# Performance work log

Measured on AMD Instinct MI355X. Metric: run time of the kernel, lower is better.

The kernel has to match this reference:

```python
import jax, jax.numpy as jnp
import numpy as np

D_MODEL = 1024
N_HEADS = 16
HEAD_DIM = D_MODEL // N_HEADS
D_FF = 4096
ROPE_RANK = 16
LN_EPS = 1e-5


def _ln(x, g, b):
    mu = jnp.mean(x, axis=-1, keepdims=True)
    var = jnp.mean((x - mu) ** 2, axis=-1, keepdims=True)
    return (x - mu) * jax.lax.rsqrt(var + LN_EPS) * g + b


def _rope(x, A, B_):
    # x: [B, T, D]; learned low-rank additive correction to sin/cos tables
    B, T, D = x.shape
    pos = jnp.arange(T, dtype=jnp.float32)
    theta = 1.0 / (10000.0 ** (jnp.arange(0, D, 2, dtype=jnp.float32) / D))  # [D/2]
    angles = pos[:, None] * theta[None, :]                                   # [T, D/2]
    sin_pos, cos_pos = jnp.sin(angles), jnp.cos(angles)
    base = jnp.concatenate([sin_pos, cos_pos], axis=-1)                      # [T, D]
    learned = (base @ A) @ B_                                                # [T, D]
    l_sin, l_cos = jnp.split(learned, 2, axis=-1)
    sin_f = sin_pos + l_sin                                                  # [T, D/2]
    cos_f = cos_pos + l_cos
    xe, xo = x[..., ::2], x[..., 1::2]
    re = xe * cos_f[None] - xo * sin_f[None]
    ro = xe * sin_f[None] + xo * cos_f[None]
    return jnp.stack([re, ro], axis=-1).reshape(B, T, D)


def setup_inputs() -> dict:
    key = jax.random.key(0)
    ks = jax.random.split(key, 20)
    B, T = 2, 2048
    s = 1.0 / np.sqrt(D_MODEL)
    sf = 1.0 / np.sqrt(D_FF)
    sr = 1.0 / np.sqrt(ROPE_RANK)
    return {
        "tgt": jax.random.normal(ks[0], (B, T, D_MODEL), jnp.float32),
        "Wq": jax.random.normal(ks[1], (D_MODEL, D_MODEL), jnp.float32) * s,
        "bq": jnp.zeros((D_MODEL,), jnp.float32),
        "Wk": jax.random.normal(ks[2], (D_MODEL, D_MODEL), jnp.float32) * s,
        "bk": jnp.zeros((D_MODEL,), jnp.float32),
        "Wv": jax.random.normal(ks[3], (D_MODEL, D_MODEL), jnp.float32) * s,
        "bv": jnp.zeros((D_MODEL,), jnp.float32),
        "Wo": jax.random.normal(ks[4], (D_MODEL, D_MODEL), jnp.float32) * s,
        "bo": jnp.zeros((D_MODEL,), jnp.float32),
        "W1": jax.random.normal(ks[5], (D_MODEL, D_FF), jnp.float32) * s,
        "b1": jnp.zeros((D_FF,), jnp.float32),
        "W2": jax.random.normal(ks[6], (D_FF, D_MODEL), jnp.float32) * sf,
        "b2": jnp.zeros((D_MODEL,), jnp.float32),
        "ln1_g": jnp.ones((D_MODEL,), jnp.float32),
        "ln1_b": jnp.zeros((D_MODEL,), jnp.float32),
        "ln2_g": jnp.ones((D_MODEL,), jnp.float32),
        "ln2_b": jnp.zeros((D_MODEL,), jnp.float32),
        "rope_A": jax.random.normal(ks[7], (D_MODEL, ROPE_RANK), jnp.float32) * s,
        "rope_B": jax.random.normal(ks[8], (ROPE_RANK, D_MODEL), jnp.float32) * sr,
    }


def reference(tgt, Wq, bq, Wk, bk, Wv, bv, Wo, bo, W1, b1, W2, b2,
              ln1_g, ln1_b, ln2_g, ln2_b, rope_A, rope_B):
    x = tgt
    B, T, D = x.shape
    q = _rope(x @ Wq + bq, rope_A, rope_B)
    k = _rope(x @ Wk + bk, rope_A, rope_B)
    v = x @ Wv + bv
    # [B, H, T, hd]
    q = q.reshape(B, T, N_HEADS, HEAD_DIM).transpose(0, 2, 1, 3)
    k = k.reshape(B, T, N_HEADS, HEAD_DIM).transpose(0, 2, 1, 3)
    v = v.reshape(B, T, N_HEADS, HEAD_DIM).transpose(0, 2, 1, 3)
    scores = jnp.einsum("bhqd,bhkd->bhqk", q, k) / np.sqrt(HEAD_DIM)
    attn = jax.nn.softmax(scores, axis=-1)  # no mask: module applies none
    ctx = jnp.einsum("bhqk,bhkd->bhqd", attn, v)
    ctx = ctx.transpose(0, 2, 1, 3).reshape(B, T, D)
    x = x + (ctx @ Wo + bo)
    x = _ln(x, ln1_g, ln1_b)
    ff = jax.nn.relu(x @ W1 + b1) @ W2 + b2
    x = _ln(x + ff, ln2_g, ln2_b)
    return x
```

## Files before the change

### kernel.cpp

```cpp
#include <hip/hip_runtime.h>
#include <math.h>

typedef unsigned short u16;
typedef unsigned int u32;
typedef __attribute__((ext_vector_type(8))) short short8v;
typedef __attribute__((ext_vector_type(4))) float f32x4;

__device__ __forceinline__ u16 f2bf(float f) {
    u32 u = __float_as_uint(f);
    u32 r = (u + 0x7fffu + ((u >> 16) & 1u)) >> 16;
    return (u16)r;
}

#define GLOAD_LDS(g, l)                                                        \
    __builtin_amdgcn_global_load_lds(                                          \
        (const __attribute__((address_space(1))) void*)(g),                    \
        (__attribute__((address_space(3))) void*)(l), 16, 0, 0)

__global__ void cast_k(const float* __restrict__ x, u16* __restrict__ y) {
    const int gid = blockIdx.x * blockDim.x + threadIdx.x;
    float4 v = ((const float4*)x)[gid];
    ushort4 o;
    o.x = f2bf(v.x); o.y = f2bf(v.y); o.z = f2bf(v.z); o.w = f2bf(v.w);
    ((ushort4*)y)[gid] = o;
}

__global__ __launch_bounds__(256) void tcast_k(const float* __restrict__ S,
                                               u16* __restrict__ Dt,
                                               int K, int N) {
    __shared__ float tile[32][33];
    const int n0 = blockIdx.x * 32, k0 = blockIdx.y * 32;
    const int tx = threadIdx.x & 31, ty = threadIdx.x >> 5;
#pragma unroll
    for (int i = 0; i < 4; i++)
        tile[ty + 8 * i][tx] = S[(size_t)(k0 + ty + 8 * i) * N + n0 + tx];
    __syncthreads();
#pragma unroll
    for (int i = 0; i < 4; i++)
        Dt[(size_t)(n0 + ty + 8 * i) * K + k0 + tx] = f2bf(tile[tx][ty + 8 * i]);
}

__global__ __launch_bounds__(256) void vtrans_k(const u16* __restrict__ vv,
                                                u16* __restrict__ Vt) {
    __shared__ u16 tile[32][33];
    const int key0 = blockIdx.x * 32, d0 = blockIdx.y * 32, bh = blockIdx.z;
    const int b = bh >> 4, h = bh & 15;
    const int tx = threadIdx.x & 31, ty = threadIdx.x >> 5;
#pragma unroll
    for (int i = 0; i < 4; i++)
        tile[ty + 8 * i][tx] =
            vv[(size_t)(b * 2048 + key0 + ty + 8 * i) * 1024 + h * 64 + d0 + tx];
    __syncthreads();
#pragma unroll
    for (int i = 0; i < 4; i++) {
        const int d = d0 + ty + 8 * i;
        const int key = key0 + tx;
        const int ksw = (key & ~63) | ((((key >> 3) & 7) ^ (d & 7)) << 3) | (key & 7);
        Vt[((size_t)bh * 64 + d) * 2048 + ksw] = tile[tx][ty + 8 * i];
    }
}

#define ROPE_LOG2C (13.287712379549449f / 512.0f)

__global__ __launch_bounds__(256) void rope1_k(const float* __restrict__ A,
                                               float* __restrict__ P) {
    __shared__ float sc[16][17];
    __shared__ float cc[16][17];
    __shared__ float Als[16][17];
    __shared__ float Alc[16][17];
    const int tid = threadIdx.x;
    const int tt = tid >> 4, rr = tid & 15;
    const int t = blockIdx.x * 16 + tt;
    float acc = 0.f;
    for (int i0 = 0; i0 < 512; i0 += 16) {
        __syncthreads();
        {
            const int i = i0 + rr;
            const float th = exp2f(-(float)i * ROPE_LOG2C);
            const float ang = (float)t * th;
            sc[tt][rr] = sinf(ang);
            cc[tt][rr] = cosf(ang);
            Als[tt][rr] = A[(i0 + tt) * 16 + rr];
            Alc[tt][rr] = A[(512 + i0 + tt) * 16 + rr];
        }
        __syncthreads();
#pragma unroll
        for (int ii = 0; ii < 16; ++ii)
            acc = fmaf(sc[tt][ii], Als[ii][rr],
                       fmaf(cc[tt][ii], Alc[ii][rr], acc));
    }
    P[t * 16 + rr] = acc;
}

__global__ void rope2_k(const float* __restrict__ P, const float* __restrict__ Bw,
                        float* __restrict__ sf, float* __restrict__ cf) {
    const int gid = blockIdx.x * blockDim.x + threadIdx.x;
    if (gid >= 2048 * 512) return;
    const int t = gid >> 9, i = gid & 511;
    float ls = 0.f, lc = 0.f;
#pragma unroll
    for (int r = 0; r < 16; ++r) {
        const float p = P[t * 16 + r];
        ls = fmaf(p, Bw[r * 1024 + i], ls);
        lc = fmaf(p, Bw[r * 1024 + 512 + i], lc);
    }
    const float th = exp2f(-(float)i * ROPE_LOG2C);
    const float ang = (float)t * th;
    sf[gid] = sinf(ang) + ls;
    cf[gid] = cosf(ang) + lc;
}

__device__ __forceinline__ void xcd_tile(int L, int xn, int rn, int rm,
                                         int& tm, int& tn) {
    const int xcd = L & 7, i = L >> 3;
    const int cx = xcd % xn, cy = xcd / xn;
    tn = cx * rn + (i % rn);
    tm = cy * rm + (i / rn);
}

enum { EP_NONE = 0, EP_RES = 2, EP_RELU = 3 };

template <int EPI, bool CBF, int BN>
__global__ __launch_bounds__(256) void mgemm_k(
    const u16* __restrict__ A, const u16* __restrict__ Bt,
    const float* __restrict__ bias, const float* __restrict__ resf,
    void* __restrict__ Cp, int M, int N, int K, int xn, int rn, int rm) {
    constexpr int NT = BN / 32;
    __shared__ u16 As[2 * 128 * 32];
    __shared__ u16 Bs[2 * BN * 32];
    const int tid = threadIdx.x;
    const int w = tid >> 6, l = tid & 63;
    const int quad = l >> 4, lr = l & 15;
    const int wr = w >> 1, wc = w & 1;
    int tm, tn;
    xcd_tile(blockIdx.x, xn, rn, rm, tm, tn);
    const int m0 = tm * 128, n0 = tn * BN;

    const int srow = w * 16 + (l >> 2);
    const int scol = (l & 3) * 8;
    const u16* ag0 = A + (size_t)(m0 + srow) * K + scol;
    const u16* ag1 = A + (size_t)(m0 + 64 + srow) * K + scol;
    const u16* bg0 = Bt + (size_t)(n0 + srow) * K + scol;
    const u16* bg1 = Bt + (size_t)(n0 + 64 + srow) * K + scol;

    f32x4 acc[4][NT];
#pragma unroll
    for (int i = 0; i < 4; i++)
#pragma unroll
        for (int j = 0; j < NT; j++) acc[i][j] = (f32x4)(0.0f);

    {
        u16* Ab = As;
        u16* Bb = Bs;
        GLOAD_LDS(ag0, Ab + w * 512);
        GLOAD_LDS(ag1, Ab + 2048 + w * 512);
        GLOAD_LDS(bg0, Bb + w * 512);
        if (BN == 128) GLOAD_LDS(bg1, Bb + 2048 + w * 512);
    }

    const int niter = K >> 5;
    for (int i = 0; i < niter; ++i) {
        __syncthreads();
        const int knext = (i + 1) << 5;
        if (knext < K) {
            u16* Ab = As + ((i + 1) & 1) * 4096;
            u16* Bb = Bs + ((i + 1) & 1) * (BN * 32);
            GLOAD_LDS(ag0 + knext, Ab + w * 512);
            GLOAD_LDS(ag1 + knext, Ab + 2048 + w * 512);
            GLOAD_LDS(bg0 + knext, Bb + w * 512);
            if (BN == 128) GLOAD_LDS(bg1 + knext, Bb + 2048 + w * 512);
        }
        const u16* Ac = As + (i & 1) * 4096;
        const u16* Bc = Bs + (i & 1) * (BN * 32);
        short8v af[4], bf[NT];
#pragma unroll
        for (int mt = 0; mt < 4; ++mt)
            af[mt] = *(const short8v*)&Ac[(wr * 64 + mt * 16 + lr) * 32 + quad * 8];
#pragma unroll
        for (int nt = 0; nt < NT; ++nt)
            bf[nt] = *(const short8v*)&Bc[(wc * (BN / 2) + nt * 16 + lr) * 32 + quad * 8];
#pragma unroll
        for (int mt = 0; mt < 4; ++mt)
#pragma unroll
            for (int nt = 0; nt < NT; ++nt)
                acc[mt][nt] = __builtin_amdgcn_mfma_f32_16x16x32_bf16(
                    af[mt], bf[nt], acc[mt][nt], 0, 0, 0);
    }

#pragma unroll
    for (int mt = 0; mt < 4; ++mt) {
#pragma unroll
        for (int nt = 0; nt < NT; ++nt) {
            const int n = n0 + wc * (BN / 2) + nt * 16 + lr;
            const float bb = bias[n];
#pragma unroll
            for (int reg = 0; reg < 4; ++reg) {
                const int m = m0 + wr * 64 + mt * 16 + quad * 4 + reg;
                float v = acc[mt][nt][reg] + bb;
                if (EPI == EP_RES) v += resf[(size_t)m * N + n];
                if (EPI == EP_RELU) v = fmaxf(v, 0.f);
                if (CBF) ((u16*)Cp)[(size_t)m * N + n] = f2bf(v);
                else     ((float*)Cp)[(size_t)m * N + n] = v;
            }
        }
    }
}

__global__ __launch_bounds__(256) void mqkv_k(
    const u16* __restrict__ A, const u16* __restrict__ Bt,
    const float* __restrict__ bq, const float* __restrict__ bk,
    const float* __restrict__ bv, const float* __restrict__ sf,
    const float* __restrict__ cf, u16* __restrict__ out) {
    const int K = 1024;
    __shared__ u16 As[2 * 128 * 32];
    __shared__ u16 Bs[2 * 128 * 32];
    const int tid = threadIdx.x;
    const int w = tid >> 6, l = tid & 63;
    const int quad = l >> 4, lr = l & 15;
    const int wr = w >> 1, wc = w & 1;
    int tm, tn;
    xcd_tile(blockIdx.x, 4, 6, 16, tm, tn);
    const int m0 = tm * 128, n0 = tn * 128;

    const int srow = w * 16 + (l >> 2);
    const int scol = (l & 3) * 8;
    const u16* ag0 = A + (size_t)(m0 + srow) * K + scol;
    const u16* ag1 = A + (size_t)(m0 + 64 + srow) * K + scol;
    const u16* bg0 = Bt + (size_t)(n0 + srow) * K + scol;
    const u16* bg1 = Bt + (size_t)(n0 + 64 + srow) * K + scol;

    f32x4 acc[4][4];
#pragma unroll
    for (int i = 0; i < 4; i++)
#pragma unroll
        for (int j = 0; j < 4; j++) acc[i][j] = (f32x4)(0.0f);

    {
        GLOAD_LDS(ag0, As + w * 512);
        GLOAD_LDS(ag1, As + 2048 + w * 512);
        GLOAD_LDS(bg0, Bs + w * 512);
        GLOAD_LDS(bg1, Bs + 2048 + w * 512);
    }
    for (int i = 0; i < 32; ++i) {
        __syncthreads();
        const int knext = (i + 1) << 5;
        if (knext < K) {
            u16* Ab = As + ((i + 1) & 1) * 4096;
            u16* Bb = Bs + ((i + 1) & 1) * 4096;
            GLOAD_LDS(ag0 + knext, Ab + w * 512);
            GLOAD_LDS(ag1 + knext, Ab + 2048 + w * 512);
            GLOAD_LDS(bg0 + knext, Bb + w * 512);
            GLOAD_LDS(bg1 + knext, Bb + 2048 + w * 512);
        }
        const u16* Ac = As + (i & 1) * 4096;
        const u16* Bc = Bs + (i & 1) * 4096;
        short8v af[4], bf[4];
#pragma unroll
        for (int mt = 0; mt < 4; ++mt)
            af[mt] = *(const short8v*)&Ac[(wr * 64 + mt * 16 + lr) * 32 + quad * 8];
#pragma unroll
        for (int nt = 0; nt < 4; ++nt)
            bf[nt] = *(const short8v*)&Bc[(wc * 64 + nt * 16 + lr) * 32 + quad * 8];
#pragma unroll
        for (int mt = 0; mt < 4; ++mt)
#pragma unroll
            for (int nt = 0; nt < 4; ++nt)
                acc[mt][nt] = __builtin_amdgcn_mfma_f32_16x16x32_bf16(
                    af[mt], bf[nt], acc[mt][nt], 0, 0, 0);
    }

    const int which = n0 >> 10;
    const float* bias = which == 0 ? bq : (which == 1 ? bk : bv);
    const bool doRope = which < 2;
    u16* Cp = out + (size_t)which * 4096 * 1024;

#pragma unroll
    for (int mt = 0; mt < 4; ++mt) {
#pragma unroll
        for (int nt = 0; nt < 4; ++nt) {
            const int n = n0 + wc * 64 + nt * 16 + lr;
            const int col = n & 1023;
            const float bb = bias[col];
#pragma unroll
            for (int reg = 0; reg < 4; ++reg) {
                const int m = m0 + wr * 64 + mt * 16 + quad * 4 + reg;
                float v = acc[mt][nt][reg] + bb;
                const float partner = __shfl_xor(v, 1);
                int colw = col;
                if (doRope) {
                    const int t = m & 2047;
                    const int fi = col >> 1;
                    const float svv = sf[t * 512 + fi];
                    const float cvv = cf[t * 512 + fi];
                    v = (col & 1) ? fmaf(partner, svv, v * cvv)
                                  : fmaf(v, cvv, -partner * svv);
                    if (which == 0) v *= 0.125f;
                    colw = (col & ~63) | ((((col >> 3) & 7) ^ (m & 7)) << 3) |
                           (col & 7);
                }
                Cp[(size_t)m * 1024 + colw] = f2bf(v);
            }
        }
    }
}

__global__ __launch_bounds__(256, 3) void mattn_k(
    const u16* __restrict__ Q, const u16* __restrict__ Kg,
    const u16* __restrict__ Vt, u16* __restrict__ O) {
    __shared__ u16 QPs[128 * 64];
    __shared__ u16 Ks[2][64 * 64];
    __shared__ u16 Vs[2][64 * 64];
    const int tid = threadIdx.x;
    const int w = tid >> 6, l = tid & 63;
    const int quad = l >> 4, lr = l & 15;
    const int L = blockIdx.x;
    const int bh = (L & 7) * 4 + ((L >> 3) & 3);
    const int b = bh >> 4, h = bh & 15;
    const int row0 = (L >> 5) * 128;
    const size_t base = (size_t)b * 2048 * 1024 + (size_t)h * 64;
    const size_t vbase = (size_t)bh * 64 * 2048;

    const int dr = l >> 3;
    const int dc = (l & 7) * 8;
    const int g0 = w * 2, g1 = g0 + 1;
    const u16* kg0 = Kg + base + (size_t)(g0 * 8 + dr) * 1024 + dc;
    const u16* kg1 = Kg + base + (size_t)(g1 * 8 + dr) * 1024 + dc;
    const u16* vg0 = Vt + vbase + (size_t)(g0 * 8 + dr) * 2048 + dc;
    const u16* vg1 = Vt + vbase + (size_t)(g1 * 8 + dr) * 2048 + dc;

#pragma unroll
    for (int j = 0; j < 4; ++j) {
        const int g = w * 4 + j;
        GLOAD_LDS(Q + base + (size_t)(row0 + g * 8 + dr) * 1024 + dc,
                  QPs + g * 512);
    }
    GLOAD_LDS(kg0, Ks[0] + g0 * 512);
    GLOAD_LDS(kg1, Ks[0] + g1 * 512);
    GLOAD_LDS(vg0, Vs[0] + g0 * 512);
    GLOAD_LDS(vg1, Vs[0] + g1 * 512);
    __syncthreads();

    const int rsw = lr & 7;
    short8v qf[2][2];
#pragma unroll
    for (int ntq = 0; ntq < 2; ++ntq) {
        const int qr = w * 32 + ntq * 16 + lr;
#pragma unroll
        for (int kh = 0; kh < 2; ++kh)
            qf[ntq][kh] = *(const short8v*)&QPs[qr * 64 +
                (((kh * 4 + quad) ^ rsw) << 3)];
    }

    f32x4 o_acc[2][4];
#pragma unroll
    for (int i = 0; i < 2; ++i)
#pragma unroll
        for (int j = 0; j < 4; ++j) o_acc[i][j] = (f32x4)(0.0f);
    float lsum[2] = {0.f, 0.f};

    for (int i = 0; i < 32; ++i) {
        __syncthreads();
        if (i + 1 < 32) {
            const size_t kro = (size_t)((i + 1) << 6) * 1024;
            const int kco = (i + 1) << 6;
            u16* Kb = Ks[(i + 1) & 1];
            u16* Vb = Vs[(i + 1) & 1];
            GLOAD_LDS(kg0 + kro, Kb + g0 * 512);
            GLOAD_LDS(kg1 + kro, Kb + g1 * 512);
            GLOAD_LDS(vg0 + kco, Vb + g0 * 512);
            GLOAD_LDS(vg1 + kco, Vb + g1 * 512);
        }
        const u16* Kc = Ks[i & 1];
        const u16* Vc = Vs[i & 1];

        f32x4 s[4][2];
#pragma unroll
        for (int mt = 0; mt < 4; ++mt)
#pragma unroll
            for (int ntq = 0; ntq < 2; ++ntq) s[mt][ntq] = (f32x4)(0.0f);
#pragma unroll
        for (int mt = 0; mt < 4; ++mt) {
            const int kr = mt * 16 + lr;
            const short8v kf0 = *(const short8v*)&Kc[kr * 64 + ((quad ^ rsw) << 3)];
            const short8v kf1 = *(const short8v*)&Kc[kr * 64 + (((quad + 4) ^ rsw) << 3)];
#pragma unroll
            for (int ntq = 0; ntq < 2; ++ntq) {
                s[mt][ntq] = __builtin_amdgcn_mfma_f32_16x16x32_bf16(
                    kf0, qf[ntq][0], s[mt][ntq], 0, 0, 0);
                s[mt][ntq] = __builtin_amdgcn_mfma_f32_16x16x32_bf16(
                    kf1, qf[ntq][1], s[mt][ntq], 0, 0, 0);
            }
        }

#pragma unroll
        for (int ntq = 0; ntq < 2; ++ntq) {
            const int prow = w * 32 + ntq * 16 + lr;
#pragma unroll
            for (int mt = 0; mt < 4; ++mt) {
                const float e0 = __expf(s[mt][ntq][0]);
                const float e1 = __expf(s[mt][ntq][1]);
                const float e2 = __expf(s[mt][ntq][2]);
                const float e3 = __expf(s[mt][ntq][3]);
                lsum[ntq] += (e0 + e1) + (e2 + e3);
                u32 p01, p23;
                asm("v_cvt_pk_bf16_f32 %0, %1, %2" : "=v"(p01) : "v"(e0), "v"(e1));
                asm("v_cvt_pk_bf16_f32 %0, %1, %2" : "=v"(p23) : "v"(e2), "v"(e3));
                uint2 pv; pv.x = p01; pv.y = p23;
                *(uint2*)&QPs[prow * 64 +
                              (((mt * 2 + (quad >> 1)) ^ rsw) << 3) +
                              (quad & 1) * 4] = pv;
            }
        }

        short8v vf[4][2];
#pragma unroll
        for (int ntd = 0; ntd < 4; ++ntd) {
            const int vr = ntd * 16 + lr;
            vf[ntd][0] = *(const short8v*)&Vc[vr * 64 + ((quad ^ rsw) << 3)];
            vf[ntd][1] = *(const short8v*)&Vc[vr * 64 + (((quad + 4) ^ rsw) << 3)];
        }
        short8v pf[2][2];
#pragma unroll
        for (int mtq = 0; mtq < 2; ++mtq) {
            const int prow = w * 32 + mtq * 16 + lr;
            pf[mtq][0] = *(const short8v*)&QPs[prow * 64 + ((quad ^ rsw) << 3)];
            pf[mtq][1] = *(const short8v*)&QPs[prow * 64 + (((quad + 4) ^ rsw) << 3)];
        }
#pragma unroll
        for (int mtq = 0; mtq < 2; ++mtq)
#pragma unroll
            for (int ntd = 0; ntd < 4; ++ntd) {
                o_acc[mtq][ntd] = __builtin_amdgcn_mfma_f32_16x16x32_bf16(
                    pf[mtq][0], vf[ntd][0], o_acc[mtq][ntd], 0, 0, 0);
                o_acc[mtq][ntd] = __builtin_amdgcn_mfma_f32_16x16x32_bf16(
                    pf[mtq][1], vf[ntd][1], o_acc[mtq][ntd], 0, 0, 0);
            }
    }

    float rden[2];
#pragma unroll
    for (int ntq = 0; ntq < 2; ++ntq) {
        float t = lsum[ntq];
        t += __shfl_xor(t, 16);
        t += __shfl_xor(t, 32);
        rden[ntq] = 1.0f / t;
    }
#pragma unroll
    for (int mtq = 0; mtq < 2; ++mtq) {
#pragma unroll
        for (int reg = 0; reg < 4; ++reg) {
            const float dsc = __shfl(rden[mtq], quad * 4 + reg);
            const int m = row0 + w * 32 + mtq * 16 + quad * 4 + reg;
#pragma unroll
            for (int ntd = 0; ntd < 4; ++ntd)
                O[base + (size_t)m * 1024 + ntd * 16 + lr] =
                    f2bf(o_acc[mtq][ntd][reg] * dsc);
        }
    }
}

__global__ __launch_bounds__(256) void ln_k(
    const float* __restrict__ X, const float* __restrict__ g,
    const float* __restrict__ bb, float* __restrict__ outf,
    u16* __restrict__ outb) {
    const int row = blockIdx.x, tid = threadIdx.x;
    const float* x = X + (size_t)row * 1024;
    float4 xv = *(const float4*)&x[tid * 4];
    float s = xv.x + xv.y + xv.z + xv.w;
    float s2 = xv.x * xv.x + xv.y * xv.y + xv.z * xv.z + xv.w * xv.w;
#pragma unroll
    for (int msk = 32; msk >= 1; msk >>= 1) {
        s += __shfl_xor(s, msk);
        s2 += __shfl_xor(s2, msk);
    }
    __shared__ float red[8];
    const int wv = tid >> 6;
    if ((tid & 63) == 0) { red[wv] = s; red[wv + 4] = s2; }
    __syncthreads();
    s = red[0] + red[1] + red[2] + red[3];
    s2 = red[4] + red[5] + red[6] + red[7];
    const float mu = s * (1.f / 1024.f);
    float var = s2 * (1.f / 1024.f) - mu * mu;
    var = fmaxf(var, 0.f);
    const float rstd = rsqrtf(var + 1e-5f);
    float4 g4 = *(const float4*)&g[tid * 4];
    float4 b4 = *(const float4*)&bb[tid * 4];
    float o0 = (xv.x - mu) * rstd * g4.x + b4.x;
    float o1 = (xv.y - mu) * rstd * g4.y + b4.y;
    float o2 = (xv.z - mu) * rstd * g4.z + b4.z;
    float o3 = (xv.w - mu) * rstd * g4.w + b4.w;
    if (outf)
        *(float4*)(outf + (size_t)row * 1024 + tid * 4) = make_float4(o0, o1, o2, o3);
    if (outb) {
        ushort4 ov;
        ov.x = f2bf(o0); ov.y = f2bf(o1); ov.z = f2bf(o2); ov.w = f2bf(o3);
        *(ushort4*)(outb + (size_t)row * 1024 + tid * 4) = ov;
    }
}

extern "C" void kernel_launch(void* const* d_in, const int* in_sizes, int n_in,
                              void* d_out, int out_size, void* d_ws, size_t ws_size,
                              hipStream_t stream) {
    const float* tgt = (const float*)d_in[0];
    const float* Wq  = (const float*)d_in[1];
    const float* bq  = (const float*)d_in[2];
    const float* Wk  = (const float*)d_in[3];
    const float* bk  = (const float*)d_in[4];
    const float* Wv  = (const float*)d_in[5];
    const float* bv  = (const float*)d_in[6];
    const float* Wo  = (const float*)d_in[7];
    const float* bo  = (const float*)d_in[8];
    const float* W1  = (const float*)d_in[9];
    const float* b1  = (const float*)d_in[10];
    const float* W2  = (const float*)d_in[11];
    const float* b2  = (const float*)d_in[12];
    const float* g1  = (const float*)d_in[13];
    const float* be1 = (const float*)d_in[14];
    const float* g2  = (const float*)d_in[15];
    const float* be2 = (const float*)d_in[16];
    const float* rA  = (const float*)d_in[17];
    const float* rB  = (const float*)d_in[18];

    const int M = 4096, D = 1024, DFF = 4096;
    const size_t MD = (size_t)M * D;
    const size_t MB = 1u << 20;
    char* wsb = (char*)d_ws;

    u16* q    = (u16*)wsb;
    u16* vv   = q + 2 * MD;
    u16* ctx  = q + 3 * MD;
    u16* h    = q;
    float* x1  = (float*)(wsb + 32 * MB);
    float* sfp = (float*)(wsb + 48 * MB);
    float* cfp = sfp + (size_t)2048 * 512;
    u16* x1b  = (u16*)sfp;
    u16* tgtb = (u16*)(wsb + 56 * MB);
    u16* Vt   = (u16*)(wsb + 56 * MB);
    u16* Wqt  = (u16*)(wsb + 64 * MB);
    u16* Wkt  = (u16*)(wsb + 66 * MB);
    u16* Wvt  = (u16*)(wsb + 68 * MB);
    u16* Wot  = (u16*)(wsb + 70 * MB);
    u16* W1t  = (u16*)(wsb + 72 * MB);
    u16* W2t  = (u16*)(wsb + 80 * MB);
    float* Pp = (float*)(wsb + 88 * MB);

    cast_k<<<dim3(4096), dim3(256), 0, stream>>>(tgt, tgtb);
    tcast_k<<<dim3(32, 32),  dim3(256), 0, stream>>>(Wq, Wqt, D, D);
    tcast_k<<<dim3(32, 32),  dim3(256), 0, stream>>>(Wk, Wkt, D, D);
    tcast_k<<<dim3(32, 32),  dim3(256), 0, stream>>>(Wv, Wvt, D, D);
    tcast_k<<<dim3(32, 32),  dim3(256), 0, stream>>>(Wo, Wot, D, D);
    tcast_k<<<dim3(128, 32), dim3(256), 0, stream>>>(W1, W1t, D, DFF);
    tcast_k<<<dim3(32, 128), dim3(256), 0, stream>>>(W2, W2t, DFF, D);
    rope1_k<<<dim3(128), dim3(256), 0, stream>>>(rA, Pp);
    rope2_k<<<dim3(4096), dim3(256), 0, stream>>>(Pp, rB, sfp, cfp);

    mqkv_k<<<dim3(768), dim3(256), 0, stream>>>(
        tgtb, Wqt, bq, bk, bv, sfp, cfp, q);

    vtrans_k<<<dim3(64, 2, 32), dim3(256), 0, stream>>>(vv, Vt);

    mattn_k<<<dim3(512), dim3(256), 0, stream>>>(q, q + MD, Vt, ctx);

    mgemm_k<EP_RES, false, 64><<<dim3(512), dim3(256), 0, stream>>>(
        ctx, Wot, bo, tgt, x1, M, D, D, 2, 8, 8);
    ln_k<<<dim3(4096), dim3(256), 0, stream>>>(x1, g1, be1, x1, x1b);
    mgemm_k<EP_RELU, true, 128><<<dim3(1024), dim3(256), 0, stream>>>(
        x1b, W1t, b1, nullptr, h, M, DFF, D, 4, 8, 16);
    mgemm_k<EP_RES, false, 64><<<dim3(512), dim3(256), 0, stream>>>(
        h, W2t, b2, x1, x1, M, D, DFF, 2, 8, 8);
    ln_k<<<dim3(4096), dim3(256), 0, stream>>>(x1, g2, be2, (float*)d_out, nullptr);

    (void)in_sizes; (void)n_in; (void)out_size; (void)ws_size;
}
```

Baseline: 459.4 us.

## Triple-buffer GEMM LDS stages with explicit waitcnt and XOR-swizzled LDS layout

```diff
diff --git a/kernel.cpp b/kernel.cpp
--- a/kernel.cpp
+++ b/kernel.cpp
@@ -16,6 +16,8 @@
     __builtin_amdgcn_global_load_lds(                                          \
         (const __attribute__((address_space(1))) void*)(g),                    \
         (__attribute__((address_space(3))) void*)(l), 16, 0, 0)
+
+#define SCHED_FENCE() __builtin_amdgcn_sched_barrier(0)
 
 __global__ void cast_k(const float* __restrict__ x, u16* __restrict__ y) {
     const int gid = blockIdx.x * blockDim.x + threadIdx.x;
@@ -126,8 +128,8 @@
     const float* __restrict__ bias, const float* __restrict__ resf,
     void* __restrict__ Cp, int M, int N, int K, int xn, int rn, int rm) {
     constexpr int NT = BN / 32;
-    __shared__ u16 As[2 * 128 * 32];
-    __shared__ u16 Bs[2 * BN * 32];
+    __shared__ u16 As[3 * 128 * 32];
+    __shared__ u16 Bs[3 * BN * 32];
     const int tid = threadIdx.x;
     const int w = tid >> 6, l = tid & 63;
     const int quad = l >> 4, lr = l & 15;
@@ -137,7 +139,7 @@
     const int m0 = tm * 128, n0 = tn * BN;
 
     const int srow = w * 16 + (l >> 2);
-    const int scol = (l & 3) * 8;
+    const int scol = (((l & 3) ^ ((l >> 3) & 3)) * 8);
     const u16* ag0 = A + (size_t)(m0 + srow) * K + scol;
     const u16* ag1 = A + (size_t)(m0 + 64 + srow) * K + scol;
     const u16* bg0 = Bt + (size_t)(n0 + srow) * K + scol;
@@ -150,41 +152,57 @@
         for (int j = 0; j < NT; j++) acc[i][j] = (f32x4)(0.0f);
 
     {
-        u16* Ab = As;
-        u16* Bb = Bs;
-        GLOAD_LDS(ag0, Ab + w * 512);
-        GLOAD_LDS(ag1, Ab + 2048 + w * 512);
-        GLOAD_LDS(bg0, Bb + w * 512);
-        if (BN == 128) GLOAD_LDS(bg1, Bb + 2048 + w * 512);
+        GLOAD_LDS(ag0, As + w * 512);
+        GLOAD_LDS(ag1, As + 2048 + w * 512);
+        GLOAD_LDS(bg0, Bs + w * 512);
+        if (BN == 128) GLOAD_LDS(bg1, Bs + 2048 + w * 512);
+        GLOAD_LDS(ag0 + 32, As + 4096 + w * 512);
+        GLOAD_LDS(ag1 + 32, As + 4096 + 2048 + w * 512);
+        GLOAD_LDS(bg0 + 32, Bs + BN * 32 + w * 512);
+        if (BN == 128) GLOAD_LDS(bg1 + 32, Bs + BN * 32 + 2048 + w * 512);
     }
 
     const int niter = K >> 5;
+    const int xsw = ((lr >> 1) & 3) << 3;
+    int bc = 0, bs = 2;
     for (int i = 0; i < niter; ++i) {
-        __syncthreads();
-        const int knext = (i + 1) << 5;
-        if (knext < K) {
-            u16* Ab = As + ((i + 1) & 1) * 4096;
-            u16* Bb = Bs + ((i + 1) & 1) * (BN * 32);
-            GLOAD_LDS(ag0 + knext, Ab + w * 512);
-            GLOAD_LDS(ag1 + knext, Ab + 2048 + w * 512);
-            GLOAD_LDS(bg0 + knext, Bb + w * 512);
-            if (BN == 128) GLOAD_LDS(bg1 + knext, Bb + 2048 + w * 512);
-        }
-        const u16* Ac = As + (i & 1) * 4096;
-        const u16* Bc = Bs + (i & 1) * (BN * 32);
+        SCHED_FENCE();
+        if (i + 1 < niter) {
+            if (BN == 128) asm volatile("s_waitcnt vmcnt(4) lgkmcnt(0)" ::: "memory");
+            else           asm volatile("s_waitcnt vmcnt(3) lgkmcnt(0)" ::: "memory");
+        } else {
+            asm volatile("s_waitcnt vmcnt(0) lgkmcnt(0)" ::: "memory");
+        }
+        __builtin_amdgcn_s_barrier();
+        SCHED_FENCE();
+        if (i + 2 < niter) {
+            const int kk = (i + 2) << 5;
+            u16* Ab = As + bs * 4096;
+            u16* Bb = Bs + bs * (BN * 32);
+            GLOAD_LDS(ag0 + kk, Ab + w * 512);
+            GLOAD_LDS(ag1 + kk, Ab + 2048 + w * 512);
+            GLOAD_LDS(bg0 + kk, Bb + w * 512);
+            if (BN == 128) GLOAD_LDS(bg1 + kk, Bb + 2048 + w * 512);
+        }
+        const u16* Ac = As + bc * 4096;
+        const u16* Bc = Bs + bc * (BN * 32);
         short8v af[4], bf[NT];
 #pragma unroll
         for (int mt = 0; mt < 4; ++mt)
-            af[mt] = *(const short8v*)&Ac[(wr * 64 + mt * 16 + lr) * 32 + quad * 8];
+            af[mt] = *(const short8v*)&Ac[(wr * 64 + mt * 16 + lr) * 32 +
+                                          ((quad << 3) ^ xsw)];
 #pragma unroll
         for (int nt = 0; nt < NT; ++nt)
-            bf[nt] = *(const short8v*)&Bc[(wc * (BN / 2) + nt * 16 + lr) * 32 + quad * 8];
+            bf[nt] = *(const short8v*)&Bc[(wc * (BN / 2) + nt * 16 + lr) * 32 +
+                                          ((quad << 3) ^ xsw)];
 #pragma unroll
         for (int mt = 0; mt < 4; ++mt)
 #pragma unroll
             for (int nt = 0; nt < NT; ++nt)
                 acc[mt][nt] = __builtin_amdgcn_mfma_f32_16x16x32_bf16(
                     af[mt], bf[nt], acc[mt][nt], 0, 0, 0);
+        bc = (bc == 2) ? 0 : bc + 1;
+        bs = (bs == 2) ? 0 : bs + 1;
     }
 
 #pragma unroll
@@ -212,8 +230,8 @@
     const float* __restrict__ bv, const float* __restrict__ sf,
     const float* __restrict__ cf, u16* __restrict__ out) {
     const int K = 1024;
-    __shared__ u16 As[2 * 128 * 32];
-    __shared__ u16 Bs[2 * 128 * 32];
+    __shared__ u16 As[3 * 128 * 32];
+    __shared__ u16 Bs[3 * 128 * 32];
     const int tid = threadIdx.x;
     const int w = tid >> 6, l = tid & 63;
     const int quad = l >> 4, lr = l & 15;
@@ -223,7 +241,7 @@
     const int m0 = tm * 128, n0 = tn * 128;
 
     const int srow = w * 16 + (l >> 2);
-    const int scol = (l & 3) * 8;
+    const int scol = (((l & 3) ^ ((l >> 3) & 3)) * 8);
     const u16* ag0 = A + (size_t)(m0 + srow) * K + scol;
     const u16* ag1 = A + (size_t)(m0 + 64 + srow) * K + scol;
     const u16* bg0 = Bt + (size_t)(n0 + srow) * K + scol;
@@ -240,33 +258,50 @@
         GLOAD_LDS(ag1, As + 2048 + w * 512);
         GLOAD_LDS(bg0, Bs + w * 512);
         GLOAD_LDS(bg1, Bs + 2048 + w * 512);
-    }
+        GLOAD_LDS(ag0 + 32, As + 4096 + w * 512);
+        GLOAD_LDS(ag1 + 32, As + 4096 + 2048 + w * 512);
+        GLOAD_LDS(bg0 + 32, Bs + 4096 + w * 512);
+        GLOAD_LDS(bg1 + 32, Bs + 4096 + 2048 + w * 512);
+    }
+    const int xsw = ((lr >> 1) & 3) << 3;
+    int bc = 0, bsb = 2;
     for (int i = 0; i < 32; ++i) {
-        __syncthreads();
-        const int knext = (i + 1) << 5;
-        if (knext < K) {
-            u16* Ab = As + ((i + 1) & 1) * 4096;
-            u16* Bb = Bs + ((i + 1) & 1) * 4096;
-            GLOAD_LDS(ag0 + knext, Ab + w * 512);
-            GLOAD_LDS(ag1 + knext, Ab + 2048 + w * 512);
-            GLOAD_LDS(bg0 + knext, Bb + w * 512);
-            GLOAD_LDS(bg1 + knext, Bb + 2048 + w * 512);
-        }
-        const u16* Ac = As + (i & 1) * 4096;
-        const u16* Bc = Bs + (i & 1) * 4096;
+        SCHED_FENCE();
+        if (i + 1 < 32) {
+            asm volatile("s_waitcnt vmcnt(4) lgkmcnt(0)" ::: "memory");
+        } else {
+            asm volatile("s_waitcnt vmcnt(0) lgkmcnt(0)" ::: "memory");
+        }
+        __builtin_amdgcn_s_barrier();
+        SCHED_FENCE();
+        if (i + 2 < 32) {
+            const int kk = (i + 2) << 5;
+            u16* Ab = As + bsb * 4096;
+            u16* Bb = Bs + bsb * 4096;
+            GLOAD_LDS(ag0 + kk, Ab + w * 512);
+            GLOAD_LDS(ag1 + kk, Ab + 2048 + w * 512);
+            GLOAD_LDS(bg0 + kk, Bb + w * 512);
+            GLOAD_LDS(bg1 + kk, Bb + 2048 + w * 512);
+        }
+        const u16* Ac = As + bc * 4096;
+        const u16* Bc = Bs + bc * 4096;
         short8v af[4], bf[4];
 #pragma unroll
         for (int mt = 0; mt < 4; ++mt)
-            af[mt] = *(const short8v*)&Ac[(wr * 64 + mt * 16 + lr) * 32 + quad * 8];
+            af[mt] = *(const short8v*)&Ac[(wr * 64 + mt * 16 + lr) * 32 +
+                                          ((quad << 3) ^ xsw)];
 #pragma unroll
         for (int nt = 0; nt < 4; ++nt)
-            bf[nt] = *(const short8v*)&Bc[(wc * 64 + nt * 16 + lr) * 32 + quad * 8];
+            bf[nt] = *(const short8v*)&Bc[(wc * 64 + nt * 16 + lr) * 32 +
+                                          ((quad << 3) ^ xsw)];
 #pragma unroll
         for (int mt = 0; mt < 4; ++mt)
 #pragma unroll
             for (int nt = 0; nt < 4; ++nt)
                 acc[mt][nt] = __builtin_amdgcn_mfma_f32_16x16x32_bf16(
                     af[mt], bf[nt], acc[mt][nt], 0, 0, 0);
+        bc = (bc == 2) ? 0 : bc + 1;
+        bsb = (bsb == 2) ? 0 : bsb + 1;
     }
 
     const int which = n0 >> 10;
```

Measured after the change: 446.5 us. 1.03x faster.
